# Kernel optimization log

Hardware: AMD Instinct MI355X
Metric: run time of the kernel (lower is better)

Reference implementation:

```python
import jax, jax.numpy as jnp
import numpy as np

EPS_H = 1.0   # smooth Heaviside / delta regularization
MAX_ITER = 10


def _chan_vese_step(phi, I, dt, lam):
    # phi, I: [B, 512, H, W]
    px = jnp.gradient(phi, axis=3)
    py = jnp.gradient(phi, axis=2)
    nrm = jnp.sqrt(px * px + py * py + 1e-8)
    curv = jnp.gradient(px / nrm, axis=3) + jnp.gradient(py / nrm, axis=2)
    # smooth Heaviside and region means (per batch, per channel)
    H = 0.5 * (1.0 + (2.0 / jnp.pi) * jnp.arctan(phi / EPS_H))
    a1 = jnp.sum(H, axis=(2, 3), keepdims=True)
    a2 = jnp.sum(1.0 - H, axis=(2, 3), keepdims=True)
    c1 = jnp.sum(I * H, axis=(2, 3), keepdims=True) / (a1 + 1e-8)
    c2 = jnp.sum(I * (1.0 - H), axis=(2, 3), keepdims=True) / (a2 + 1e-8)
    delta = (EPS_H / jnp.pi) / (phi * phi + EPS_H * EPS_H)
    force = curv - lam * (I - c1) ** 2 + lam * (I - c2) ** 2
    return phi + dt * delta * force


def setup_inputs() -> dict:
    key = jax.random.key(0)
    ks = jax.random.split(key, 6)
    B, C, Hh, Ww = 8, 256, 64, 64
    contour = jax.random.normal(ks[0], (B, C, Hh, Ww), dtype=jnp.float32)
    g = jax.random.normal(ks[1], (B, C, Hh, Ww), dtype=jnp.float32)
    x = jax.random.normal(ks[2], (B, 2 * C, Hh, Ww), dtype=jnp.float32)
    dt = jnp.array([0.1], dtype=jnp.float32)
    lambda_ = jnp.array([1.0], dtype=jnp.float32)
    # 1x1 conv weights (no bias), stored as [out_ch, in_ch]
    g_w = jax.random.normal(ks[3], (512, C), dtype=jnp.float32) / np.sqrt(C)
    x_w = jax.random.normal(ks[4], (512, 2 * C), dtype=jnp.float32) / np.sqrt(2 * C)
    c_w = jax.random.normal(ks[5], (512, C), dtype=jnp.float32) / np.sqrt(C)
    return {"contour": contour, "g": g, "x": x, "dt": dt, "lambda_": lambda_,
            "g_w": g_w, "x_w": x_w, "c_w": c_w}


def reference(contour, g, x, dt, lambda_, g_w, x_w, c_w):
    # z = relu(g_conv(g)) + x_conv(x); 1x1 convs are per-pixel GEMMs
    z = jax.nn.relu(jnp.einsum('bchw,oc->bohw', g, g_w)) \
        + jnp.einsum('bchw,oc->bohw', x, x_w)
    phi0 = jnp.einsum('bchw,oc->bohw', contour, c_w)
    # bicubic resize of phi0 to z's spatial size is identity (same H, W)
    dts = dt[0]
    lam = lambda_[0]
    def step(phi, _):
        return _chan_vese_step(phi, z, dts, lam), None
    phi, _ = jax.lax.scan(step, phi0, None, length=MAX_ITER)
    return jax.nn.sigmoid(phi)
```

## Files before the change

### kernel.cpp

```cpp
#include <hip/hip_runtime.h>
#include <math.h>

#define PIX 4096
#define O_CH 512
#define CV_PITCH 68
#define CV_SSTR 16
#define NY_PITCH 36

#define WOFF_G 0
#define WOFF_X 131072
#define WOFF_C 393216
#define W_ELEMS 524288

typedef __attribute__((ext_vector_type(8))) short s16x8;
typedef __attribute__((ext_vector_type(4))) float f32x4;
typedef __attribute__((ext_vector_type(2))) float f32x2;

__device__ __forceinline__ unsigned cvt_pk_bf16(float a, float b) {
  unsigned r;
  asm("v_cvt_pk_bf16_f32 %0, %1, %2" : "=v"(r) : "v"(a), "v"(b));
  return r;
}

__global__ __launch_bounds__(256) void conv_w(
    const float* __restrict__ gw, const float* __restrict__ xw,
    const float* __restrict__ cw,
    ushort* __restrict__ WH, ushort* __restrict__ WL)
{
  const int r = blockIdx.y;
  const float* src = (r == 0) ? gw : ((r == 1) ? xw : cw);
  const int n4 = (r == 1) ? 65536 : 32768;
  const int doff = (r == 0) ? WOFF_G : ((r == 1) ? WOFF_X : WOFF_C);
  const int i = blockIdx.x * 256 + threadIdx.x;
  if (i >= n4) return;
  float4 v = ((const float4*)src)[i];
  unsigned h01 = cvt_pk_bf16(v.x, v.y);
  unsigned h23 = cvt_pk_bf16(v.z, v.w);
  float l0 = v.x - __uint_as_float(h01 << 16);
  float l1 = v.y - __uint_as_float(h01 & 0xffff0000u);
  float l2 = v.z - __uint_as_float(h23 << 16);
  float l3 = v.w - __uint_as_float(h23 & 0xffff0000u);
  unsigned lo01 = cvt_pk_bf16(l0, l1);
  unsigned lo23 = cvt_pk_bf16(l2, l3);
  ((uint2*)(WH + doff))[i] = make_uint2(h01, h23);
  ((uint2*)(WL + doff))[i] = make_uint2(lo01, lo23);
}

__global__ __launch_bounds__(256, 2) void mfma_gemm_all(
    const float* __restrict__ g, const float* __restrict__ x,
    const float* __restrict__ contour,
    const ushort* __restrict__ WHg, const ushort* __restrict__ WLg,
    float* __restrict__ z, float* __restrict__ phi0)
{
  __shared__ ushort WHs[8192], WLs[8192], AHs[8192], ALs[8192];
  const int t = threadIdx.x;
  const int lane = t & 63, wave = t >> 6;
  const int wm = wave >> 1, wn = wave & 1;
  const int rowA = lane & 15, kg = lane >> 4;
  const int pb = blockIdx.x * 128, ob = blockIdx.y * 128;
  const int bz = blockIdx.z;
  const bool isZ = bz < 8;
  const int b = isZ ? bz : bz - 8;

  const int woff1 = isZ ? WOFF_G : WOFF_C;
  const float* A1 = (isZ ? g : contour) + (size_t)b * 256 * PIX;
  const float* A2 = x + (size_t)(isZ ? b : 0) * 512 * PIX;
  float* out = (isZ ? z : phi0) + (size_t)b * O_CH * PIX;
  const int nsteps = isZ ? 12 : 4;

  f32x4 acc[4][4];
#pragma unroll
  for (int mi = 0; mi < 4; ++mi)
#pragma unroll
    for (int ni = 0; ni < 4; ++ni) acc[mi][ni] = (f32x4){0.f, 0.f, 0.f, 0.f};

  float pf[2][2][8];

#pragma unroll
  for (int ph = 0; ph < 2; ++ph) {
    const float* acp = A1 + pb + ph * 64 + lane;
#pragma unroll
    for (int ch = 0; ch < 2; ++ch) {
      const int kl0 = ch * 32 + wave * 8;
#pragma unroll
      for (int j = 0; j < 8; ++j)
        pf[ph][ch][j] = acp[(size_t)(kl0 + j) * PIX];
    }
  }

  for (int st = 0; st < nsteps; ++st) {
    const bool s2 = st >= 4;
    const int K = s2 ? 512 : 256;
    const int woff = s2 ? WOFF_X : woff1;
    const int kb = (s2 ? st - 4 : st) * 64;

    {
      const int o_r = t >> 1, hf = t & 1;
      const size_t wbase = (size_t)woff + (size_t)(ob + o_r) * K + kb + hf * 32;
      const ushort* whrow = WHg + wbase;
      const ushort* wlrow = WLg + wbase;
#pragma unroll
      for (int i = 0; i < 4; ++i) {
        int idx = o_r * 64 + (((hf * 4 + i) ^ (o_r & 7)) << 3);
        *(s16x8*)&WHs[idx] = *(const s16x8*)(whrow + i * 8);
        *(s16x8*)&WLs[idx] = *(const s16x8*)(wlrow + i * 8);
      }
    }
#pragma unroll
    for (int ph = 0; ph < 2; ++ph) {
      const int rp = ph * 64 + lane;
#pragma unroll
      for (int ch = 0; ch < 2; ++ch) {
        unsigned h[4], l[4];
#pragma unroll
        for (int j2 = 0; j2 < 4; ++j2) {
          float v0 = pf[ph][ch][2 * j2], v1 = pf[ph][ch][2 * j2 + 1];
          h[j2] = cvt_pk_bf16(v0, v1);
          float lo0 = v0 - __uint_as_float(h[j2] << 16);
          float lo1 = v1 - __uint_as_float(h[j2] & 0xffff0000u);
          l[j2] = cvt_pk_bf16(lo0, lo1);
        }
        int grp = ch * 4 + wave;
        int idx = rp * 64 + ((grp ^ (rp & 7)) << 3);
        *(uint4*)&AHs[idx] = make_uint4(h[0], h[1], h[2], h[3]);
        *(uint4*)&ALs[idx] = make_uint4(l[0], l[1], l[2], l[3]);
      }
    }
    __syncthreads();

    if (st + 1 < nsteps) {
      const bool n2 = (st + 1) >= 4;
      const float* Ab = n2 ? A2 : A1;
      const int kbn = (n2 ? st + 1 - 4 : st + 1) * 64;
#pragma unroll
      for (int ph = 0; ph < 2; ++ph) {
        const float* acp = Ab + (size_t)kbn * PIX + pb + ph * 64 + lane;
#pragma unroll
        for (int ch = 0; ch < 2; ++ch) {
          const int kl0 = ch * 32 + wave * 8;
#pragma unroll
          for (int j = 0; j < 8; ++j)
            pf[ph][ch][j] = acp[(size_t)(kl0 + j) * PIX];
        }
      }
    }

#pragma unroll
    for (int ks = 0; ks < 2; ++ks) {
      s16x8 wh[4], wlv[4], ah[4], alv[4];
#pragma unroll
      for (int mi = 0; mi < 4; ++mi) {
        int row = wm * 64 + mi * 16 + rowA;
        int idx = row * 64 + (((ks * 4 + kg) ^ (row & 7)) << 3);
        wh[mi]  = *(const s16x8*)&WHs[idx];
        wlv[mi] = *(const s16x8*)&WLs[idx];
      }
#pragma unroll
      for (int ni = 0; ni < 4; ++ni) {
        int row = wn * 64 + ni * 16 + rowA;
        int idx = row * 64 + (((ks * 4 + kg) ^ (row & 7)) << 3);
        ah[ni]  = *(const s16x8*)&AHs[idx];
        alv[ni] = *(const s16x8*)&ALs[idx];
      }
#pragma unroll
      for (int mi = 0; mi < 4; ++mi)
#pragma unroll
        for (int ni = 0; ni < 4; ++ni) {
          acc[mi][ni] = __builtin_amdgcn_mfma_f32_16x16x32_bf16(wh[mi],  ah[ni],  acc[mi][ni], 0, 0, 0);
          acc[mi][ni] = __builtin_amdgcn_mfma_f32_16x16x32_bf16(wh[mi],  alv[ni], acc[mi][ni], 0, 0, 0);
          acc[mi][ni] = __builtin_amdgcn_mfma_f32_16x16x32_bf16(wlv[mi], ah[ni],  acc[mi][ni], 0, 0, 0);
        }
    }
    if (isZ && st == 3) {
#pragma unroll
      for (int mi = 0; mi < 4; ++mi)
#pragma unroll
        for (int ni = 0; ni < 4; ++ni)
#pragma unroll
          for (int r = 0; r < 4; ++r) acc[mi][ni][r] = fmaxf(acc[mi][ni][r], 0.f);
    }
    __syncthreads();
  }

  const int orow = (lane >> 4) * 4, pcol = lane & 15;
#pragma unroll
  for (int mi = 0; mi < 4; ++mi)
#pragma unroll
    for (int ni = 0; ni < 4; ++ni)
#pragma unroll
      for (int r = 0; r < 4; ++r)
        out[(size_t)(ob + wm * 64 + mi * 16 + orow + r) * PIX +
            pb + wn * 64 + ni * 16 + pcol] = acc[mi][ni][r];
}

__device__ __forceinline__ float fast_atan(float x) {
  float a = __builtin_fabsf(x);
  float inv = __builtin_amdgcn_rcpf(a);
  bool big = a > 1.f;
  float tt = big ? inv : a;
  float t2 = tt * tt;
  float p = fmaf(t2, 0.0208351f, -0.0851330f);
  p = fmaf(t2, p, 0.1801410f);
  p = fmaf(t2, p, -0.3302995f);
  p = fmaf(t2, p, 0.9998660f);
  p = p * tt;
  float r = big ? (1.57079632679f - p) : p;
  return __builtin_copysignf(r, x);
}

__global__ __launch_bounds__(256, 4) void chanvese(
    const float* __restrict__ zb, float* __restrict__ ob,
    const float* __restrict__ dtp, const float* __restrict__ lamp)
{
  __shared__ float phi_l[64 * CV_PITCH];
  __shared__ unsigned ny_l[64 * NY_PITCH];
  __shared__ float red[12];
  const int t = threadIdx.x;
  const int lane = t & 63, wv = t >> 6;
  const int row = t >> 2, s = t & 3;
  const size_t gbase = (size_t)blockIdx.x * PIX + row * 64 + s * 16;
  const float dtv = dtp[0], lam = lamp[0];
  const float INV_PI = 0.31830988618379067f;
  const float dtpi = dtv * INV_PI;
  const float fy = (row == 0 || row == 63) ? 1.f : 0.5f;
  const float exl = (s == 0) ? 2.f : 1.f;
  const float exr = (s == 3) ? 2.f : 1.f;
  const int my  = row * CV_PITCH + s * CV_SSTR;
  const int ub  = ((row == 0) ? 0 : row - 1) * CV_PITCH + s * CV_SSTR;
  const int db  = ((row == 63) ? 63 : row + 1) * CV_PITCH + s * CV_SSTR;
  const int myn = row * NY_PITCH + s * 8;
  const int ubn = ((row == 0) ? 0 : row - 1) * NY_PITCH + s * 8;
  const int dbn = ((row == 63) ? 63 : row + 1) * NY_PITCH + s * 8;
  const f32x2 eps2 = {1e-8f, 1e-8f};

  f32x2 I2[8], ph2[8], nx2[8];
#pragma unroll
  for (int q = 0; q < 4; ++q) {
    f32x4 iv = *(const f32x4*)(zb + gbase + q * 4);
    f32x4 pv = *(const f32x4*)(ob + gbase + q * 4);
    I2[2 * q]     = (f32x2){iv[0], iv[1]};
    I2[2 * q + 1] = (f32x2){iv[2], iv[3]};
    ph2[2 * q]     = (f32x2){pv[0], pv[1]};
    ph2[2 * q + 1] = (f32x2){pv[2], pv[3]};
    *(f32x4*)&phi_l[my + q * 4] = pv;
  }
  float sI = 0.f, s_at = 0.f, s_iat = 0.f;
#pragma unroll
  for (int p = 0; p < 8; ++p) {
    sI += I2[p].x + I2[p].y;
    float a0 = fast_atan(ph2[p].x), a1 = fast_atan(ph2[p].y);
    s_at += a0 + a1;
    s_iat = fmaf(I2[p].x, a0, fmaf(I2[p].y, a1, s_iat));
  }
#pragma unroll
  for (int off = 32; off; off >>= 1) {
    sI += __shfl_xor(sI, off);
    s_at += __shfl_xor(s_at, off);
    s_iat += __shfl_xor(s_iat, off);
  }
  if (lane == 0) { red[wv] = s_at; red[4 + wv] = s_iat; red[8 + wv] = sI; }
  __syncthreads();
  float S_at = red[0] + red[1] + red[2] + red[3];
  float S_iat = red[4] + red[5] + red[6] + red[7];
  const float sumI = red[8] + red[9] + red[10] + red[11];

  for (int it = 0; it < 10; ++it) {
    float a1 = fmaf(INV_PI, S_at, 2048.f);
    float sIH = fmaf(INV_PI, S_iat, 0.5f * sumI);
    float c1 = sIH * __builtin_amdgcn_rcpf(a1 + 1e-8f);
    float c2 = (sumI - sIH) * __builtin_amdgcn_rcpf(4096.f - a1 + 1e-8f);
    float lam12 = lam * (c1 - c2);
    float ms12 = -(c1 + c2);

    float ls = __shfl(ph2[7].y, lane - 1);
    float rs = __shfl(ph2[0].x, lane + 1);
    float lb = (s == 0) ? ph2[0].x : ls;
    float rb = (s == 3) ? ph2[7].y : rs;
    unsigned nyp[8];
#pragma unroll
    for (int q = 0; q < 4; ++q) {
      f32x4 uv = *(const f32x4*)&phi_l[ub + q * 4];
      f32x4 dv = *(const f32x4*)&phi_l[db + q * 4];
#pragma unroll
      for (int e = 0; e < 2; ++e) {
        const int p = 2 * q + e;
        f32x2 u2 = (f32x2){uv[2 * e], uv[2 * e + 1]};
        f32x2 d2 = (f32x2){dv[2 * e], dv[2 * e + 1]};
        f32x2 py = (d2 - u2) * fy;
        f32x2 L = {(p == 0) ? lb : ph2[p - 1].y, ph2[p].x};
        f32x2 R = {ph2[p].y, (p == 7) ? rb : ph2[p + 1].x};
        f32x2 px = (R - L) * 0.5f;
        if (p == 0) px.x *= exl;
        if (p == 7) px.y *= exr;
        f32x2 qq = px * px + (py * py + eps2);
        f32x2 rn = {__builtin_amdgcn_rsqf(qq.x), __builtin_amdgcn_rsqf(qq.y)};
        nx2[p] = px * rn;
        f32x2 nyv = py * rn;
        nyp[p] = cvt_pk_bf16(nyv.x, nyv.y);
      }
    }
    *(uint4*)&ny_l[myn]     = make_uint4(nyp[0], nyp[1], nyp[2], nyp[3]);
    *(uint4*)&ny_l[myn + 4] = make_uint4(nyp[4], nyp[5], nyp[6], nyp[7]);
    __syncthreads();

    float nls = __shfl(nx2[7].y, lane - 1);
    float nrs = __shfl(nx2[0].x, lane + 1);
    float nlb = (s == 0) ? nx2[0].x : nls;
    float nrb = (s == 3) ? nx2[7].y : nrs;
    f32x2 inc_at2 = {0.f, 0.f}, inc_iat2 = {0.f, 0.f};
#pragma unroll
    for (int h = 0; h < 2; ++h) {
      uint4 au = *(const uint4*)&ny_l[ubn + 4 * h];
      uint4 ad = *(const uint4*)&ny_l[dbn + 4 * h];
      unsigned ua[4] = {au.x, au.y, au.z, au.w};
      unsigned ud[4] = {ad.x, ad.y, ad.z, ad.w};
      f32x2 phs[4];
#pragma unroll
      for (int e = 0; e < 4; ++e) {
        const int p = 4 * h + e;
        f32x2 nyu = {__uint_as_float(ua[e] << 16), __uint_as_float(ua[e] & 0xffff0000u)};
        f32x2 nyd = {__uint_as_float(ud[e] << 16), __uint_as_float(ud[e] & 0xffff0000u)};
        f32x2 dny = (nyd - nyu) * fy;
        f32x2 L = {(p == 0) ? nlb : nx2[p - 1].y, nx2[p].x};
        f32x2 R = {nx2[p].y, (p == 7) ? nrb : nx2[p + 1].x};
        f32x2 dnx = (R - L) * 0.5f;
        if (p == 0) dnx.x *= exl;
        if (p == 7) dnx.y *= exr;
        f32x2 curv = dnx + dny;
        f32x2 c = ph2[p];
        f32x2 den = c * c + (f32x2){1.f, 1.f};
        f32x2 rcd = {__builtin_amdgcn_rcpf(den.x), __builtin_amdgcn_rcpf(den.y)};
        f32x2 tI = I2[p] * 2.f + (f32x2){ms12, ms12};
        f32x2 force = tI * lam12 + curv;
        f32x2 dphi = (rcd * dtpi) * force;
        f32x2 pn = c + dphi;
        ph2[p] = pn;
        phs[e] = pn;
        f32x2 da = dphi * rcd;
        inc_at2 += da;
        inc_iat2 = I2[p] * da + inc_iat2;
      }
      if (it < 9) {
        *(f32x4*)&phi_l[my + 8 * h] =
            (f32x4){phs[0].x, phs[0].y, phs[1].x, phs[1].y};
        *(f32x4*)&phi_l[my + 8 * h + 4] =
            (f32x4){phs[2].x, phs[2].y, phs[3].x, phs[3].y};
      }
    }
    if (it < 9) {
      float inc_at = inc_at2.x + inc_at2.y;
      float inc_iat = inc_iat2.x + inc_iat2.y;
#pragma unroll
      for (int off = 32; off; off >>= 1) {
        inc_at += __shfl_xor(inc_at, off);
        inc_iat += __shfl_xor(inc_iat, off);
      }
      if (lane == 0) { red[2 * wv] = inc_at; red[2 * wv + 1] = inc_iat; }
      __syncthreads();
      S_at += red[0] + red[2] + red[4] + red[6];
      S_iat += red[1] + red[3] + red[5] + red[7];
    }
  }

#pragma unroll
  for (int q = 0; q < 4; ++q) {
    f32x2 pa = ph2[2 * q], pb2 = ph2[2 * q + 1];
    float o0 = 1.f / (1.f + exp2f(pa.x * -1.44269504089f));
    float o1 = 1.f / (1.f + exp2f(pa.y * -1.44269504089f));
    float o2 = 1.f / (1.f + exp2f(pb2.x * -1.44269504089f));
    float o3 = 1.f / (1.f + exp2f(pb2.y * -1.44269504089f));
    *(float4*)(ob + gbase + q * 4) = make_float4(o0, o1, o2, o3);
  }
}

extern "C" void kernel_launch(void* const* d_in, const int* in_sizes, int n_in,
                              void* d_out, int out_size, void* d_ws, size_t ws_size,
                              hipStream_t stream)
{
  const float* contour = (const float*)d_in[0];
  const float* g       = (const float*)d_in[1];
  const float* x       = (const float*)d_in[2];
  const float* dt      = (const float*)d_in[3];
  const float* lam     = (const float*)d_in[4];
  const float* g_w     = (const float*)d_in[5];
  const float* x_w     = (const float*)d_in[6];
  const float* c_w     = (const float*)d_in[7];
  float* out = (float*)d_out;
  float* z   = (float*)d_ws;
  ushort* WH = (ushort*)(z + (size_t)8 * O_CH * PIX);
  ushort* WL = WH + W_ELEMS;

  conv_w<<<dim3(256, 3), dim3(256), 0, stream>>>(g_w, x_w, c_w, WH, WL);
  mfma_gemm_all<<<dim3(32, 4, 16), dim3(256), 0, stream>>>(
      g, x, contour, WH, WL, z, out);
  chanvese<<<dim3(4096), dim3(256), 0, stream>>>(z, out, dt, lam);
}
```

Measured before the change: 248.8 us.

## Use 512 threads per Chan-Vese block with 8 pixels each and fp32 ny

Doubles the threads per image block in the Chan-Vese kernel so each thread handles 8 pixels instead of 16, and stores the normalized y-gradient in shared memory as fp32 instead of packed bf16. The goal is more parallelism and latency hiding per image, plus dropping the bf16 pack/unpack work and its precision loss. In exchange the block-level reductions now combine 8 waves instead of 4, barriers span more waves, and the ny shared buffer grows, which may limit how many blocks fit per CU.

```diff
diff --git a/kernel.cpp b/kernel.cpp
--- a/kernel.cpp
+++ b/kernel.cpp
@@ -4,8 +4,6 @@
 #define PIX 4096
 #define O_CH 512
 #define CV_PITCH 68
-#define CV_SSTR 16
-#define NY_PITCH 36
 
 #define WOFF_G 0
 #define WOFF_X 131072
@@ -208,34 +206,32 @@
   return __builtin_copysignf(r, x);
 }
 
-__global__ __launch_bounds__(256, 4) void chanvese(
+__global__ __launch_bounds__(512, 4) void chanvese(
     const float* __restrict__ zb, float* __restrict__ ob,
     const float* __restrict__ dtp, const float* __restrict__ lamp)
 {
   __shared__ float phi_l[64 * CV_PITCH];
-  __shared__ unsigned ny_l[64 * NY_PITCH];
-  __shared__ float red[12];
+  __shared__ float ny_l[64 * CV_PITCH];
+  __shared__ float red[24];
   const int t = threadIdx.x;
   const int lane = t & 63, wv = t >> 6;
-  const int row = t >> 2, s = t & 3;
-  const size_t gbase = (size_t)blockIdx.x * PIX + row * 64 + s * 16;
+  const int row = t >> 3, s = t & 7;
+  const int col0 = s * 8;
+  const size_t gbase = (size_t)blockIdx.x * PIX + row * 64 + col0;
   const float dtv = dtp[0], lam = lamp[0];
   const float INV_PI = 0.31830988618379067f;
   const float dtpi = dtv * INV_PI;
   const float fy = (row == 0 || row == 63) ? 1.f : 0.5f;
   const float exl = (s == 0) ? 2.f : 1.f;
-  const float exr = (s == 3) ? 2.f : 1.f;
-  const int my  = row * CV_PITCH + s * CV_SSTR;
-  const int ub  = ((row == 0) ? 0 : row - 1) * CV_PITCH + s * CV_SSTR;
-  const int db  = ((row == 63) ? 63 : row + 1) * CV_PITCH + s * CV_SSTR;
-  const int myn = row * NY_PITCH + s * 8;
-  const int ubn = ((row == 0) ? 0 : row - 1) * NY_PITCH + s * 8;
-  const int dbn = ((row == 63) ? 63 : row + 1) * NY_PITCH + s * 8;
+  const float exr = (s == 7) ? 2.f : 1.f;
+  const int my = row * CV_PITCH + col0;
+  const int ub = ((row == 0) ? 0 : row - 1) * CV_PITCH + col0;
+  const int db = ((row == 63) ? 63 : row + 1) * CV_PITCH + col0;
   const f32x2 eps2 = {1e-8f, 1e-8f};
 
-  f32x2 I2[8], ph2[8], nx2[8];
-#pragma unroll
-  for (int q = 0; q < 4; ++q) {
+  f32x2 I2[4], ph2[4], nx2[4];
+#pragma unroll
+  for (int q = 0; q < 2; ++q) {
     f32x4 iv = *(const f32x4*)(zb + gbase + q * 4);
     f32x4 pv = *(const f32x4*)(ob + gbase + q * 4);
     I2[2 * q]     = (f32x2){iv[0], iv[1]};
@@ -246,7 +242,7 @@
   }
   float sI = 0.f, s_at = 0.f, s_iat = 0.f;
 #pragma unroll
-  for (int p = 0; p < 8; ++p) {
+  for (int p = 0; p < 4; ++p) {
     sI += I2[p].x + I2[p].y;
     float a0 = fast_atan(ph2[p].x), a1 = fast_atan(ph2[p].y);
     s_at += a0 + a1;
@@ -258,11 +254,15 @@
     s_at += __shfl_xor(s_at, off);
     s_iat += __shfl_xor(s_iat, off);
   }
-  if (lane == 0) { red[wv] = s_at; red[4 + wv] = s_iat; red[8 + wv] = sI; }
+  if (lane == 0) { red[wv] = s_at; red[8 + wv] = s_iat; red[16 + wv] = sI; }
   __syncthreads();
-  float S_at = red[0] + red[1] + red[2] + red[3];
-  float S_iat = red[4] + red[5] + red[6] + red[7];
-  const float sumI = red[8] + red[9] + red[10] + red[11];
+  float S_at = 0.f, S_iat = 0.f, sumI = 0.f;
+#pragma unroll
+  for (int w = 0; w < 8; ++w) {
+    S_at += red[w];
+    S_iat += red[8 + w];
+    sumI += red[16 + w];
+  }
 
   for (int it = 0; it < 10; ++it) {
     float a1 = fmaf(INV_PI, S_at, 2048.f);
@@ -272,15 +272,15 @@
     float lam12 = lam * (c1 - c2);
     float ms12 = -(c1 + c2);
 
-    float ls = __shfl(ph2[7].y, lane - 1);
+    float ls = __shfl(ph2[3].y, lane - 1);
     float rs = __shfl(ph2[0].x, lane + 1);
     float lb = (s == 0) ? ph2[0].x : ls;
-    float rb = (s == 3) ? ph2[7].y : rs;
-    unsigned nyp[8];
-#pragma unroll
-    for (int q = 0; q < 4; ++q) {
+    float rb = (s == 7) ? ph2[3].y : rs;
+#pragma unroll
+    for (int q = 0; q < 2; ++q) {
       f32x4 uv = *(const f32x4*)&phi_l[ub + q * 4];
       f32x4 dv = *(const f32x4*)&phi_l[db + q * 4];
+      f32x4 nyo;
 #pragma unroll
       for (int e = 0; e < 2; ++e) {
         const int p = 2 * q + e;
@@ -288,44 +288,42 @@
         f32x2 d2 = (f32x2){dv[2 * e], dv[2 * e + 1]};
         f32x2 py = (d2 - u2) * fy;
         f32x2 L = {(p == 0) ? lb : ph2[p - 1].y, ph2[p].x};
-        f32x2 R = {ph2[p].y, (p == 7) ? rb : ph2[p + 1].x};
+        f32x2 R = {ph2[p].y, (p == 3) ? rb : ph2[p + 1].x};
         f32x2 px = (R - L) * 0.5f;
         if (p == 0) px.x *= exl;
-        if (p == 7) px.y *= exr;
+        if (p == 3) px.y *= exr;
         f32x2 qq = px * px + (py * py + eps2);
         f32x2 rn = {__builtin_amdgcn_rsqf(qq.x), __builtin_amdgcn_rsqf(qq.y)};
         nx2[p] = px * rn;
         f32x2 nyv = py * rn;
-        nyp[p] = cvt_pk_bf16(nyv.x, nyv.y);
-      }
-    }
-    *(uint4*)&ny_l[myn]     = make_uint4(nyp[0], nyp[1], nyp[2], nyp[3]);
-    *(uint4*)&ny_l[myn + 4] = make_uint4(nyp[4], nyp[5], nyp[6], nyp[7]);
+        nyo[2 * e] = nyv.x;
+        nyo[2 * e + 1] = nyv.y;
+      }
+      *(f32x4*)&ny_l[my + q * 4] = nyo;
+    }
     __syncthreads();
 
-    float nls = __shfl(nx2[7].y, lane - 1);
+    float nls = __shfl(nx2[3].y, lane - 1);
     float nrs = __shfl(nx2[0].x, lane + 1);
     float nlb = (s == 0) ? nx2[0].x : nls;
-    float nrb = (s == 3) ? nx2[7].y : nrs;
+    float nrb = (s == 7) ? nx2[3].y : nrs;
     f32x2 inc_at2 = {0.f, 0.f}, inc_iat2 = {0.f, 0.f};
 #pragma unroll
-    for (int h = 0; h < 2; ++h) {
-      uint4 au = *(const uint4*)&ny_l[ubn + 4 * h];
-      uint4 ad = *(const uint4*)&ny_l[dbn + 4 * h];
-      unsigned ua[4] = {au.x, au.y, au.z, au.w};
-      unsigned ud[4] = {ad.x, ad.y, ad.z, ad.w};
-      f32x2 phs[4];
-#pragma unroll
-      for (int e = 0; e < 4; ++e) {
-        const int p = 4 * h + e;
-        f32x2 nyu = {__uint_as_float(ua[e] << 16), __uint_as_float(ua[e] & 0xffff0000u)};
-        f32x2 nyd = {__uint_as_float(ud[e] << 16), __uint_as_float(ud[e] & 0xffff0000u)};
+    for (int q = 0; q < 2; ++q) {
+      f32x4 au = *(const f32x4*)&ny_l[ub + q * 4];
+      f32x4 ad = *(const f32x4*)&ny_l[db + q * 4];
+      f32x4 pho;
+#pragma unroll
+      for (int e = 0; e < 2; ++e) {
+        const int p = 2 * q + e;
+        f32x2 nyu = (f32x2){au[2 * e], au[2 * e + 1]};
+        f32x2 nyd = (f32x2){ad[2 * e], ad[2 * e + 1]};
         f32x2 dny = (nyd - nyu) * fy;
         f32x2 L = {(p == 0) ? nlb : nx2[p - 1].y, nx2[p].x};
-        f32x2 R = {nx2[p].y, (p == 7) ? nrb : nx2[p + 1].x};
+        f32x2 R = {nx2[p].y, (p == 3) ? nrb : nx2[p + 1].x};
         f32x2 dnx = (R - L) * 0.5f;
         if (p == 0) dnx.x *= exl;
-        if (p == 7) dnx.y *= exr;
+        if (p == 3) dnx.y *= exr;
         f32x2 curv = dnx + dny;
         f32x2 c = ph2[p];
         f32x2 den = c * c + (f32x2){1.f, 1.f};
@@ -335,17 +333,13 @@
         f32x2 dphi = (rcd * dtpi) * force;
         f32x2 pn = c + dphi;
         ph2[p] = pn;
-        phs[e] = pn;
+        pho[2 * e] = pn.x;
+        pho[2 * e + 1] = pn.y;
         f32x2 da = dphi * rcd;
         inc_at2 += da;
         inc_iat2 = I2[p] * da + inc_iat2;
       }
-      if (it < 9) {
-        *(f32x4*)&phi_l[my + 8 * h] =
-            (f32x4){phs[0].x, phs[0].y, phs[1].x, phs[1].y};
-        *(f32x4*)&phi_l[my + 8 * h + 4] =
-            (f32x4){phs[2].x, phs[2].y, phs[3].x, phs[3].y};
-      }
+      if (it < 9) *(f32x4*)&phi_l[my + q * 4] = pho;
     }
     if (it < 9) {
       float inc_at = inc_at2.x + inc_at2.y;
@@ -357,13 +351,16 @@
       }
       if (lane == 0) { red[2 * wv] = inc_at; red[2 * wv + 1] = inc_iat; }
       __syncthreads();
-      S_at += red[0] + red[2] + red[4] + red[6];
-      S_iat += red[1] + red[3] + red[5] + red[7];
-    }
-  }
-
-#pragma unroll
-  for (int q = 0; q < 4; ++q) {
+#pragma unroll
+      for (int w = 0; w < 8; ++w) {
+        S_at += red[2 * w];
+        S_iat += red[2 * w + 1];
+      }
+    }
+  }
+
+#pragma unroll
+  for (int q = 0; q < 2; ++q) {
     f32x2 pa = ph2[2 * q], pb2 = ph2[2 * q + 1];
     float o0 = 1.f / (1.f + exp2f(pa.x * -1.44269504089f));
     float o1 = 1.f / (1.f + exp2f(pa.y * -1.44269504089f));
@@ -393,5 +390,5 @@
   conv_w<<<dim3(256, 3), dim3(256), 0, stream>>>(g_w, x_w, c_w, WH, WL);
   mfma_gemm_all<<<dim3(32, 4, 16), dim3(256), 0, stream>>>(
       g, x, contour, WH, WL, z, out);
-  chanvese<<<dim3(4096), dim3(256), 0, stream>>>(z, out, dt, lam);
-}
+  chanvese<<<dim3(4096), dim3(512), 0, stream>>>(z, out, dt, lam);
+}
```

Measured after the change: 287.8 us. 15.7% more time.
